# Performance work log

Measured on AMD Instinct MI355X. Metric: run time of the kernel, lower is better.

The kernel has to match this reference:

```python
import jax, jax.numpy as jnp
import numpy as np

NEG = 16          # negative_samples
SKIP = 1          # skip_step


def setup_inputs() -> dict:
    key = jax.random.key(0)
    k1, k2, k3, k4 = jax.random.split(key, 4)
    B, C, H, Wd = 16, 256, 32, 32
    K = 5
    maxN = (H - SKIP - 1) * Wd * B          # largest y'*x*B (k=1)
    z = jax.random.normal(k1, (B, C, H, Wd), dtype=jnp.float32)
    c = jax.random.normal(k2, (B, C, H, Wd), dtype=jnp.float32)
    # 1x1 conv weights W_k: [K, out, in]; scaled so scores are O(1)
    W = jax.random.normal(k3, (K, C, C), dtype=jnp.float32) * (1.0 / C)
    rand_index = jax.random.randint(k4, (K, maxN * NEG), 0, maxN, dtype=jnp.int32)
    return {"z": z, "c": c, "W": W, "rand_index": rand_index}


def reference(z, c, W, rand_index):
    # CLAPP/CPC hinge contrastive loss, contrast_mode='hinge', gating=None,
    # which_update='both', no_gamma=False.
    K = W.shape[0]
    total_loss = jnp.float32(0.0)
    for k in range(1, K + 1):
        # ztwk = W_k(z[:, :, k+skip:, :]) permuted to [y, x, B, C]
        zt = z[:, :, k + SKIP:, :]                              # [B, C, y, x]
        ztwk = jnp.einsum('bcyx,oc->yxbo', zt, W[k - 1])        # [y, x, B, O]
        y, x, b, o = ztwk.shape
        N = y * x * b
        # negative sampling: gather NEG random rows of flattened ztwk
        flat = ztwk.reshape(N, o)
        idx = rand_index[k - 1, :N * NEG] % N                   # in-range indices
        ztwk_shuf = flat[idx].reshape(y, x, b, NEG, o)          # [y, x, B, neg, C]
        # context = c[:, :, :-(k+skip), :] permuted to [y, x, B, C]
        ctx = jnp.transpose(c[:, :, :-(k + SKIP), :], (2, 3, 0, 1))
        scores_pos = jnp.einsum('yxbc,yxbc->yxb', ctx, ztwk)            # [y, x, B]
        scores_neg = jnp.einsum('yxbc,yxbnc->yxbn', ctx, ztwk_shuf)     # [y, x, B, neg]
        # CLAPPHingeLoss (no_gamma=False): clamped hinge terms
        losses_pos = jnp.where(scores_pos < 1.0, 1.0 - scores_pos, 0.0)
        losses_neg = jnp.where(scores_neg > -1.0, 1.0 + scores_neg, 0.0)
        # per-sample means over (neg, y, x) then mean over batch; pos is
        # replicated over neg in the original, which leaves the mean unchanged
        loss_k = losses_pos.mean(axis=(0, 1)).mean() + losses_neg.mean(axis=(0, 1, 3)).mean()
        total_loss = total_loss + loss_k
    return total_loss
```

## Files before the change

### kernel.cpp

```cpp
#include <hip/hip_runtime.h>


typedef unsigned short u16;
typedef unsigned char u8;
typedef unsigned int u32;
typedef __attribute__((ext_vector_type(8))) short bf16x8;
typedef __attribute__((ext_vector_type(4))) float f32x4;
typedef __attribute__((ext_vector_type(2))) float f32x2;

#define NEG_  16
#define MAXN_ 15360
#define TOTROWS 71680
#define NSCORE 17920
#define NPOSP  1200
#define NPARTS (NSCORE + NPOSP)

__device__ __forceinline__ u16 f2bf(float f) {
    union { u32 i; float f; } v; v.f = f;
    u32 b = v.i;
    return (u16)((b + 0x7FFFu + ((b >> 16) & 1u)) >> 16);
}

__device__ __forceinline__ size_t frag_addr(int row, int k) {
    return ((size_t)(row >> 4) * 8 + (k >> 5)) * 512
         + (size_t)((row & 15) + 16 * ((k >> 3) & 3)) * 8 + (k & 7);
}

__global__ __launch_bounds__(256) void transpose_kernel(
    const float* __restrict__ z, const float* __restrict__ cc,
    const float* __restrict__ W,
    u16* __restrict__ ztr, u8* __restrict__ ct8, u16* __restrict__ Wbf)
{
    int tid = threadIdx.x;
    if (blockIdx.z == 2) {
        if (blockIdx.y != 0 || blockIdx.x >= 320) return;
        int i4 = blockIdx.x * 256 + tid;
        float4 v = reinterpret_cast<const float4*>(W)[i4];
        int e = i4 * 4;
        int kw = e >> 16;
        int rem = e & 65535;
        int o = rem >> 8, c = rem & 255;
        size_t base = (size_t)kw * 65536 + frag_addr(o, c);
        ushort4 u;
        u.x = f2bf(v.x); u.y = f2bf(v.y); u.z = f2bf(v.z); u.w = f2bf(v.w);
        *reinterpret_cast<ushort4*>(Wbf + base) = u;
        return;
    }
    int by = blockIdx.x;
    int b = by >> 5, y = by & 31;
    int c0 = blockIdx.y * 64;
    bool is_c = (blockIdx.z == 1);
    if (is_c && y >= 30) return;
    const float* src = is_c ? cc : z;

    __shared__ float ts[64][33];
    int x = tid & 31, ci0 = tid >> 5;
#pragma unroll
    for (int i = 0; i < 8; ++i) {
        int ci = ci0 + i * 8;
        ts[ci][x] = src[(((size_t)b * 256 + c0 + ci) * 32 + y) * 32 + x];
    }
    __syncthreads();
    int cw = tid & 63, xw0 = tid >> 6;
    if (is_c) {
#pragma unroll
        for (int i = 0; i < 8; ++i) {
            int xw = xw0 + i * 4;
            float v = ts[cw][xw];
            u32 pk = __builtin_amdgcn_cvt_pk_fp8_f32(v, v, 0, false);
            ct8[(((size_t)y * 32 + xw) * 16 + b) * 256 + c0 + cw] = (u8)pk;
        }
    } else {
        int k = c0 + cw;
#pragma unroll
        for (int i = 0; i < 8; ++i) {
            int xw = xw0 + i * 4;
            int row = (y * 32 + xw) * 16 + b;
            ztr[frag_addr(row, k)] = f2bf(ts[cw][xw]);
        }
    }
}

__global__ __launch_bounds__(256) void gemm_mfma_kernel(
    const u16* __restrict__ ztr, const u16* __restrict__ Wbf,
    const u8* __restrict__ ct8,
    u8* __restrict__ ztwk8, float* __restrict__ posPart)
{
    int kidx = blockIdx.y;
    int rowTiles = (30 - kidx) * 8;
    if ((int)blockIdx.x >= rowTiles) {
        if (threadIdx.x == 0) posPart[kidx * 240 + blockIdx.x] = 0.f;
        return;
    }
    int row0 = blockIdx.x * 64;
    int offk = 512 * (30 * kidx - (kidx * (kidx - 1)) / 2);

    int tile0 = (((kidx + 2) * 512 + row0) >> 4);
    const u16* Bsw = Wbf + (size_t)kidx * 65536;
    u8* out = ztwk8 + ((size_t)offk + row0) * 256;

    int wid = threadIdx.x >> 6, lane = threadIdx.x & 63;
    int col0 = wid * 64;

    f32x4 acc[4][4] = {};

    for (int kb = 0; kb < 8; ++kb) {
        bf16x8 a[4], b[4];
#pragma unroll
        for (int i = 0; i < 4; ++i)
            a[i] = *reinterpret_cast<const bf16x8*>(
                ztr + ((size_t)(tile0 + i) * 8 + kb) * 512 + lane * 8);
#pragma unroll
        for (int j = 0; j < 4; ++j)
            b[j] = *reinterpret_cast<const bf16x8*>(
                Bsw + ((size_t)(wid * 4 + j) * 8 + kb) * 512 + lane * 8);
#pragma unroll
        for (int i = 0; i < 4; ++i)
#pragma unroll
            for (int j = 0; j < 4; ++j)
                acc[i][j] = __builtin_amdgcn_mfma_f32_16x16x32_bf16(b[j], a[i], acc[i][j], 0, 0, 0);
    }

    int lr = lane & 15;
    int rq = (lane >> 4) * 4;
    __shared__ float pos[4][64];

#pragma unroll
    for (int i = 0; i < 4; ++i) {
        int local = row0 + i * 16 + lr;
        float pp = 0.f;
#pragma unroll
        for (int j = 0; j < 4; ++j) {
            u32 u = 0;
            u = __builtin_amdgcn_cvt_pk_fp8_f32(acc[i][j][0], acc[i][j][1], u, false);
            u = __builtin_amdgcn_cvt_pk_fp8_f32(acc[i][j][2], acc[i][j][3], u, true);
            *reinterpret_cast<u32*>(out + (size_t)(i * 16 + lr) * 256 + col0 + j * 16 + rq) = u;
            u32 cw_ = *reinterpret_cast<const u32*>(ct8 + (size_t)local * 256 + col0 + j * 16 + rq);
            f32x2 clo = __builtin_amdgcn_cvt_pk_f32_fp8(cw_, false);
            f32x2 chi = __builtin_amdgcn_cvt_pk_f32_fp8(cw_, true);
            pp = fmaf(acc[i][j][0], clo.x, pp);
            pp = fmaf(acc[i][j][1], clo.y, pp);
            pp = fmaf(acc[i][j][2], chi.x, pp);
            pp = fmaf(acc[i][j][3], chi.y, pp);
        }
        pp += __shfl_xor(pp, 16);
        pp += __shfl_xor(pp, 32);
        if (lane < 16) pos[wid][i * 16 + lane] = pp;
    }
    __syncthreads();

    if (threadIdx.x < 64) {
        float p = pos[0][threadIdx.x] + pos[1][threadIdx.x]
                + pos[2][threadIdx.x] + pos[3][threadIdx.x];
        float Nk = (float)((30 - kidx) * 512);
        float h = fmaxf(0.f, 1.f - p) / Nk;
#pragma unroll
        for (int s = 1; s < 64; s <<= 1) h += __shfl_xor(h, s);
        if (threadIdx.x == 0) posPart[kidx * 240 + blockIdx.x] = h;
    }
}

__device__ __forceinline__ float dot16(uint4 nb, const f32x2* cp) {
    f32x2 d0 = {0.f, 0.f}, d1 = {0.f, 0.f};
    d0 += __builtin_amdgcn_cvt_pk_f32_fp8(nb.x, false) * cp[0];
    d1 += __builtin_amdgcn_cvt_pk_f32_fp8(nb.x, true)  * cp[1];
    d0 += __builtin_amdgcn_cvt_pk_f32_fp8(nb.y, false) * cp[2];
    d1 += __builtin_amdgcn_cvt_pk_f32_fp8(nb.y, true)  * cp[3];
    d0 += __builtin_amdgcn_cvt_pk_f32_fp8(nb.z, false) * cp[4];
    d1 += __builtin_amdgcn_cvt_pk_f32_fp8(nb.z, true)  * cp[5];
    d0 += __builtin_amdgcn_cvt_pk_f32_fp8(nb.w, false) * cp[6];
    d1 += __builtin_amdgcn_cvt_pk_f32_fp8(nb.w, true)  * cp[7];
    f32x2 d = d0 + d1;
    return d.x + d.y;
}

__global__ __launch_bounds__(256) void score_kernel(
    const u8* __restrict__ ztwk8, const u8* __restrict__ ct8,
    const int* __restrict__ rind, float* __restrict__ partials)
{
    __shared__ float red[4];
    int bid = blockIdx.x;
    int swb = (bid & 7) * 2240 + (bid >> 3);
    int wid = threadIdx.x >> 6, lane = threadIdx.x & 63;
    int gp = swb * 4 + wid;

    const int ends0 = 15360, ends1 = 30208, ends2 = 44544, ends3 = 58368;
    int kidx, off;
    if (gp < ends0)      { kidx = 0; off = 0; }
    else if (gp < ends1) { kidx = 1; off = ends0; }
    else if (gp < ends2) { kidx = 2; off = ends1; }
    else if (gp < ends3) { kidx = 3; off = ends2; }
    else                 { kidx = 4; off = ends3; }
    int Nk = (30 - kidx) * 512;
    int local = gp - off;

    int r = lane >> 4, c16 = lane & 15;

    const int* rbase = rind + (size_t)kidx * (MAXN_ * NEG_) + (size_t)local * NEG_ + r;
    int rv0 = rbase[0], rv1 = rbase[4], rv2 = rbase[8], rv3 = rbase[12];
    int i0 = rv0 >= Nk ? rv0 - Nk : rv0;
    int i1 = rv1 >= Nk ? rv1 - Nk : rv1;
    int i2 = rv2 >= Nk ? rv2 - Nk : rv2;
    int i3 = rv3 >= Nk ? rv3 - Nk : rv3;

    const u8* zb = ztwk8 + (size_t)off * 256 + c16 * 16;
    uint4 nb0 = *reinterpret_cast<const uint4*>(zb + (size_t)i0 * 256);
    uint4 nb1 = *reinterpret_cast<const uint4*>(zb + (size_t)i1 * 256);
    uint4 nb2 = *reinterpret_cast<const uint4*>(zb + (size_t)i2 * 256);
    uint4 nb3 = *reinterpret_cast<const uint4*>(zb + (size_t)i3 * 256);

    uint4 cw4 = *reinterpret_cast<const uint4*>(ct8 + (size_t)local * 256 + c16 * 16);
    f32x2 cp[8];
    cp[0] = __builtin_amdgcn_cvt_pk_f32_fp8(cw4.x, false);
    cp[1] = __builtin_amdgcn_cvt_pk_f32_fp8(cw4.x, true);
    cp[2] = __builtin_amdgcn_cvt_pk_f32_fp8(cw4.y, false);
    cp[3] = __builtin_amdgcn_cvt_pk_f32_fp8(cw4.y, true);
    cp[4] = __builtin_amdgcn_cvt_pk_f32_fp8(cw4.z, false);
    cp[5] = __builtin_amdgcn_cvt_pk_f32_fp8(cw4.z, true);
    cp[6] = __builtin_amdgcn_cvt_pk_f32_fp8(cw4.w, false);
    cp[7] = __builtin_amdgcn_cvt_pk_f32_fp8(cw4.w, true);

    float d, h = 0.f;
    d = dot16(nb0, cp);
    d += __shfl_xor(d, 1); d += __shfl_xor(d, 2);
    d += __shfl_xor(d, 4); d += __shfl_xor(d, 8);
    h += fmaxf(0.f, 1.f + d);
    d = dot16(nb1, cp);
    d += __shfl_xor(d, 1); d += __shfl_xor(d, 2);
    d += __shfl_xor(d, 4); d += __shfl_xor(d, 8);
    h += fmaxf(0.f, 1.f + d);
    d = dot16(nb2, cp);
    d += __shfl_xor(d, 1); d += __shfl_xor(d, 2);
    d += __shfl_xor(d, 4); d += __shfl_xor(d, 8);
    h += fmaxf(0.f, 1.f + d);
    d = dot16(nb3, cp);
    d += __shfl_xor(d, 1); d += __shfl_xor(d, 2);
    d += __shfl_xor(d, 4); d += __shfl_xor(d, 8);
    h += fmaxf(0.f, 1.f + d);

    float val = h * (1.0f / 16.0f);
    val += __shfl_xor(val, 16);
    val += __shfl_xor(val, 32);
    val *= 1.0f / (float)Nk;

    if (lane == 0) red[wid] = val;
    __syncthreads();
    if (threadIdx.x == 0)
        partials[bid] = red[0] + red[1] + red[2] + red[3];
}

__global__ __launch_bounds__(256) void reduce1_kernel(
    const float* __restrict__ comb, float* __restrict__ r1)
{
    __shared__ float s[256];
    float a = 0.f;
    for (int i = blockIdx.x * 256 + threadIdx.x; i < NPARTS; i += 64 * 256)
        a += comb[i];
    s[threadIdx.x] = a;
    __syncthreads();
    for (int st = 128; st > 0; st >>= 1) {
        if ((int)threadIdx.x < st) s[threadIdx.x] += s[threadIdx.x + st];
        __syncthreads();
    }
    if (threadIdx.x == 0) r1[blockIdx.x] = s[0];
}

__global__ __launch_bounds__(64) void reduce2_kernel(
    const float* __restrict__ r1, float* __restrict__ out)
{
    float a = r1[threadIdx.x];
#pragma unroll
    for (int s = 1; s < 64; s <<= 1) a += __shfl_xor(a, s);
    if (threadIdx.x == 0) out[0] = a;
}

extern "C" void kernel_launch(void* const* d_in, const int* in_sizes, int n_in,
                              void* d_out, int out_size, void* d_ws, size_t ws_size,
                              hipStream_t stream) {
    const float* z    = (const float*)d_in[0];
    const float* c    = (const float*)d_in[1];
    const float* W    = (const float*)d_in[2];
    const int*   rind = (const int*)d_in[3];

    char* ws = (char*)d_ws;
    u16*   ztr     = (u16*)  (ws + 0);
    u8*    ct8     = (u8*)   (ws + 8388608);
    u8*    ztwk8   = (u8*)   (ws + 12320768);
    float* parts   = (float*)(ws + 30670848);
    float* posPart = (float*)(ws + 30742528);
    float* r1      = (float*)(ws + 30747328);
    u16*   Wbf     = (u16*)  (ws + 30747648);
    float* out     = (float*)d_out;

    transpose_kernel<<<dim3(512, 4, 3), 256, 0, stream>>>(z, c, W, ztr, ct8, Wbf);
    gemm_mfma_kernel<<<dim3(240, 5), 256, 0, stream>>>(ztr, Wbf, ct8, ztwk8, posPart);
    score_kernel<<<dim3(NSCORE), 256, 0, stream>>>(ztwk8, ct8, rind, parts);
    reduce1_kernel<<<dim3(64), 256, 0, stream>>>(parts, r1);
    reduce2_kernel<<<dim3(1), 64, 0, stream>>>(r1, out);
}
```

Baseline: 71.11 us.

## Compact GEMM grid, double-buffer MFMA loads, interleave score shuffles, merge reductions

The GEMM launch now uses a flat 1120-block grid that maps each block to its k-slice, so the idle early-exit blocks are gone. The operand fragments are register double-buffered, so the next k-step's loads are issued before the current MFMAs. The score kernel interleaves the four independent shuffle reductions to expose more ILP. The two final reduction kernels become one 1024-thread kernel, saving a launch. The trade-off is higher register pressure in the GEMM from the extra buffers.

```diff
diff --git a/kernel.cpp b/kernel.cpp
--- a/kernel.cpp
+++ b/kernel.cpp
@@ -12,7 +12,7 @@
 #define MAXN_ 15360
 #define TOTROWS 71680
 #define NSCORE 17920
-#define NPOSP  1200
+#define NPOSP  1120
 #define NPARTS (NSCORE + NPOSP)
 
 __device__ __forceinline__ u16 f2bf(float f) {
@@ -86,13 +86,14 @@
     const u8* __restrict__ ct8,
     u8* __restrict__ ztwk8, float* __restrict__ posPart)
 {
-    int kidx = blockIdx.y;
-    int rowTiles = (30 - kidx) * 8;
-    if ((int)blockIdx.x >= rowTiles) {
-        if (threadIdx.x == 0) posPart[kidx * 240 + blockIdx.x] = 0.f;
-        return;
-    }
-    int row0 = blockIdx.x * 64;
+    int flat = blockIdx.x;
+    int kidx, base;
+    if (flat < 240)      { kidx = 0; base = 0; }
+    else if (flat < 472) { kidx = 1; base = 240; }
+    else if (flat < 696) { kidx = 2; base = 472; }
+    else if (flat < 912) { kidx = 3; base = 696; }
+    else                 { kidx = 4; base = 912; }
+    int row0 = (flat - base) * 64;
     int offk = 512 * (30 * kidx - (kidx * (kidx - 1)) / 2);
 
     int tile0 = (((kidx + 2) * 512 + row0) >> 4);
@@ -102,23 +103,41 @@
     int wid = threadIdx.x >> 6, lane = threadIdx.x & 63;
     int col0 = wid * 64;
 
+    const u16* Abase = ztr + (size_t)tile0 * 8 * 512 + lane * 8;
+    const u16* Bbase = Bsw + (size_t)wid * 4 * 8 * 512 + lane * 8;
+
     f32x4 acc[4][4] = {};
-
+    bf16x8 a[4], b[4];
+
+#pragma unroll
+    for (int i = 0; i < 4; ++i)
+        a[i] = *reinterpret_cast<const bf16x8*>(Abase + (size_t)i * 8 * 512);
+#pragma unroll
+    for (int j = 0; j < 4; ++j)
+        b[j] = *reinterpret_cast<const bf16x8*>(Bbase + (size_t)j * 8 * 512);
+
+#pragma unroll
     for (int kb = 0; kb < 8; ++kb) {
-        bf16x8 a[4], b[4];
-#pragma unroll
-        for (int i = 0; i < 4; ++i)
-            a[i] = *reinterpret_cast<const bf16x8*>(
-                ztr + ((size_t)(tile0 + i) * 8 + kb) * 512 + lane * 8);
-#pragma unroll
-        for (int j = 0; j < 4; ++j)
-            b[j] = *reinterpret_cast<const bf16x8*>(
-                Bsw + ((size_t)(wid * 4 + j) * 8 + kb) * 512 + lane * 8);
+        bf16x8 a2[4], b2[4];
+        if (kb < 7) {
+#pragma unroll
+            for (int i = 0; i < 4; ++i)
+                a2[i] = *reinterpret_cast<const bf16x8*>(Abase + ((size_t)i * 8 + kb + 1) * 512);
+#pragma unroll
+            for (int j = 0; j < 4; ++j)
+                b2[j] = *reinterpret_cast<const bf16x8*>(Bbase + ((size_t)j * 8 + kb + 1) * 512);
+        }
 #pragma unroll
         for (int i = 0; i < 4; ++i)
 #pragma unroll
             for (int j = 0; j < 4; ++j)
                 acc[i][j] = __builtin_amdgcn_mfma_f32_16x16x32_bf16(b[j], a[i], acc[i][j], 0, 0, 0);
+        if (kb < 7) {
+#pragma unroll
+            for (int i = 0; i < 4; ++i) a[i] = a2[i];
+#pragma unroll
+            for (int j = 0; j < 4; ++j) b[j] = b2[j];
+        }
     }
 
     int lr = lane & 15;
@@ -156,7 +175,7 @@
         float h = fmaxf(0.f, 1.f - p) / Nk;
 #pragma unroll
         for (int s = 1; s < 64; s <<= 1) h += __shfl_xor(h, s);
-        if (threadIdx.x == 0) posPart[kidx * 240 + blockIdx.x] = h;
+        if (threadIdx.x == 0) posPart[flat] = h;
     }
 }
 
@@ -220,23 +239,22 @@
     cp[6] = __builtin_amdgcn_cvt_pk_f32_fp8(cw4.w, false);
     cp[7] = __builtin_amdgcn_cvt_pk_f32_fp8(cw4.w, true);
 
-    float d, h = 0.f;
-    d = dot16(nb0, cp);
-    d += __shfl_xor(d, 1); d += __shfl_xor(d, 2);
-    d += __shfl_xor(d, 4); d += __shfl_xor(d, 8);
-    h += fmaxf(0.f, 1.f + d);
-    d = dot16(nb1, cp);
-    d += __shfl_xor(d, 1); d += __shfl_xor(d, 2);
-    d += __shfl_xor(d, 4); d += __shfl_xor(d, 8);
-    h += fmaxf(0.f, 1.f + d);
-    d = dot16(nb2, cp);
-    d += __shfl_xor(d, 1); d += __shfl_xor(d, 2);
-    d += __shfl_xor(d, 4); d += __shfl_xor(d, 8);
-    h += fmaxf(0.f, 1.f + d);
-    d = dot16(nb3, cp);
-    d += __shfl_xor(d, 1); d += __shfl_xor(d, 2);
-    d += __shfl_xor(d, 4); d += __shfl_xor(d, 8);
-    h += fmaxf(0.f, 1.f + d);
+    float d0 = dot16(nb0, cp);
+    float d1 = dot16(nb1, cp);
+    float d2 = dot16(nb2, cp);
+    float d3 = dot16(nb3, cp);
+
+    d0 += __shfl_xor(d0, 1); d1 += __shfl_xor(d1, 1);
+    d2 += __shfl_xor(d2, 1); d3 += __shfl_xor(d3, 1);
+    d0 += __shfl_xor(d0, 2); d1 += __shfl_xor(d1, 2);
+    d2 += __shfl_xor(d2, 2); d3 += __shfl_xor(d3, 2);
+    d0 += __shfl_xor(d0, 4); d1 += __shfl_xor(d1, 4);
+    d2 += __shfl_xor(d2, 4); d3 += __shfl_xor(d3, 4);
+    d0 += __shfl_xor(d0, 8); d1 += __shfl_xor(d1, 8);
+    d2 += __shfl_xor(d2, 8); d3 += __shfl_xor(d3, 8);
+
+    float h = fmaxf(0.f, 1.f + d0) + fmaxf(0.f, 1.f + d1)
+            + fmaxf(0.f, 1.f + d2) + fmaxf(0.f, 1.f + d3);
 
     float val = h * (1.0f / 16.0f);
     val += __shfl_xor(val, 16);
@@ -249,29 +267,23 @@
         partials[bid] = red[0] + red[1] + red[2] + red[3];
 }
 
-__global__ __launch_bounds__(256) void reduce1_kernel(
-    const float* __restrict__ comb, float* __restrict__ r1)
+__global__ __launch_bounds__(1024) void reduce_kernel(
+    const float* __restrict__ comb, float* __restrict__ out)
 {
-    __shared__ float s[256];
+    __shared__ float s[16];
     float a = 0.f;
-    for (int i = blockIdx.x * 256 + threadIdx.x; i < NPARTS; i += 64 * 256)
-        a += comb[i];
-    s[threadIdx.x] = a;
+    for (int i = threadIdx.x; i < NPARTS; i += 1024) a += comb[i];
+#pragma unroll
+    for (int t = 1; t < 64; t <<= 1) a += __shfl_xor(a, t);
+    int w = threadIdx.x >> 6, lane = threadIdx.x & 63;
+    if (lane == 0) s[w] = a;
     __syncthreads();
-    for (int st = 128; st > 0; st >>= 1) {
-        if ((int)threadIdx.x < st) s[threadIdx.x] += s[threadIdx.x + st];
-        __syncthreads();
-    }
-    if (threadIdx.x == 0) r1[blockIdx.x] = s[0];
-}
-
-__global__ __launch_bounds__(64) void reduce2_kernel(
-    const float* __restrict__ r1, float* __restrict__ out)
-{
-    float a = r1[threadIdx.x];
-#pragma unroll
-    for (int s = 1; s < 64; s <<= 1) a += __shfl_xor(a, s);
-    if (threadIdx.x == 0) out[0] = a;
+    if (threadIdx.x < 16) {
+        float v = s[threadIdx.x];
+#pragma unroll
+        for (int t = 1; t < 16; t <<= 1) v += __shfl_xor(v, t);
+        if (threadIdx.x == 0) out[0] = v;
+    }
 }
 
 extern "C" void kernel_launch(void* const* d_in, const int* in_sizes, int n_in,
@@ -288,13 +300,11 @@
     u8*    ztwk8   = (u8*)   (ws + 12320768);
     float* parts   = (float*)(ws + 30670848);
     float* posPart = (float*)(ws + 30742528);
-    float* r1      = (float*)(ws + 30747328);
-    u16*   Wbf     = (u16*)  (ws + 30747648);
+    u16*   Wbf     = (u16*)  (ws + 30747008);
     float* out     = (float*)d_out;
 
     transpose_kernel<<<dim3(512, 4, 3), 256, 0, stream>>>(z, c, W, ztr, ct8, Wbf);
-    gemm_mfma_kernel<<<dim3(240, 5), 256, 0, stream>>>(ztr, Wbf, ct8, ztwk8, posPart);
+    gemm_mfma_kernel<<<dim3(NPOSP), 256, 0, stream>>>(ztr, Wbf, ct8, ztwk8, posPart);
     score_kernel<<<dim3(NSCORE), 256, 0, stream>>>(ztwk8, ct8, rind, parts);
-    reduce1_kernel<<<dim3(64), 256, 0, stream>>>(parts, r1);
-    reduce2_kernel<<<dim3(1), 64, 0, stream>>>(r1, out);
-}
+    reduce_kernel<<<dim3(1), 1024, 0, stream>>>(parts, out);
+}
```

New measurement: 72.29 us. Within noise of the previous version (+1.6%).
